# Performance work log

Measured on AMD Instinct MI355X. Metric: run time of the kernel, lower is better.

## Reference

```python
import jax, jax.numpy as jnp
import numpy as np

EMB = 1024
HEADS = 16
HEAD_DIM = EMB // HEADS


def setup_inputs() -> dict:
    key = jax.random.key(0)
    ks = jax.random.split(key, 5)
    x = jax.random.normal(ks[0], (4, 2048, EMB), dtype=jnp.float32)
    # qkv Linear: weight [3*EMB, EMB] in torch; store transposed for x @ W
    Wqkv = jax.random.normal(ks[1], (EMB, 3 * EMB), dtype=jnp.float32) * (1.0 / np.sqrt(EMB))
    bqkv = jax.random.normal(ks[2], (3 * EMB,), dtype=jnp.float32) * 0.01
    Wout = jax.random.normal(ks[3], (EMB, EMB), dtype=jnp.float32) * (1.0 / np.sqrt(EMB))
    bout = jax.random.normal(ks[4], (EMB,), dtype=jnp.float32) * 0.01
    return {"x": x, "Wqkv": Wqkv, "bqkv": bqkv, "Wout": Wout, "bout": bout}


def reference(x, Wqkv, bqkv, Wout, bout):
    B, N, _ = x.shape
    qkv = x @ Wqkv + bqkv                              # [B, N, 3*EMB]
    qkv = qkv.reshape(B, N, 3, HEADS, HEAD_DIM)
    q, k, v = jnp.moveaxis(qkv, 2, 0)                  # each [B, N, H, D]
    q = jnp.swapaxes(q, 1, 2)                          # [B, H, N, D]
    k = jnp.swapaxes(k, 1, 2)
    v = jnp.swapaxes(v, 1, 2)
    scale = 1.0 / np.sqrt(HEAD_DIM).astype(np.float32)
    scores = jnp.einsum('bhqd,bhkd->bhqk', q, k) * scale
    attn = jax.nn.softmax(scores, axis=-1)             # dropout p=0 (eval)
    out = jnp.einsum('bhqk,bhkd->bhqd', attn, v)       # [B, H, N, D]
    out = jnp.swapaxes(out, 1, 2).reshape(B, N, EMB)
    return out @ Wout + bout
```

## Files before the change

### kernel.cpp

```cpp
#include <hip/hip_runtime.h>

#define SEQ   2048
#define EMBD  1024
#define HEADS 16
#define HDIM  64
#define MTOT  8192
#define LOG2E 1.44269504f

typedef __attribute__((ext_vector_type(8))) _Float16 half8;
typedef __attribute__((ext_vector_type(4))) _Float16 half4;
typedef __attribute__((ext_vector_type(2))) __fp16 fp16x2;
typedef __attribute__((ext_vector_type(4))) float f32x4;

__device__ __forceinline__ f32x4 mfma16(half8 a, half8 b, f32x4 c) {
  return __builtin_amdgcn_mfma_f32_16x16x32_f16(a, b, c, 0, 0, 0);
}

__device__ __forceinline__ void gload_lds16(const void* g, void* l) {
  __builtin_amdgcn_global_load_lds(
      (const __attribute__((address_space(1))) unsigned int*)g,
      (__attribute__((address_space(3))) unsigned int*)l, 16, 0, 0);
}

__global__ void k_cvt(const float* __restrict__ in, _Float16* __restrict__ out) {
  size_t i = (size_t)blockIdx.x * blockDim.x + threadIdx.x;
  const f32x4* in4 = (const f32x4*)in;
  f32x4 a = in4[2 * i], b = in4[2 * i + 1];
  half8 h;
  h[0] = (_Float16)a[0]; h[1] = (_Float16)a[1];
  h[2] = (_Float16)a[2]; h[3] = (_Float16)a[3];
  h[4] = (_Float16)b[0]; h[5] = (_Float16)b[1];
  h[6] = (_Float16)b[2]; h[7] = (_Float16)b[3];
  *(half8*)(out + i * 8) = h;
}

__global__ __launch_bounds__(256) void k_transpose(const float* __restrict__ in,
                                                   _Float16* __restrict__ out,
                                                   int R, int C) {
  __shared__ _Float16 tile[64][65];
  const int tid = threadIdx.x;
  const int r0 = blockIdx.y * 64, c0 = blockIdx.x * 64;
  const int tr = tid >> 6;
  const int tc = tid & 63;
  #pragma unroll
  for (int i = 0; i < 16; ++i) {
    const int r = i * 4 + tr;
    tile[r][tc] = (_Float16)in[(size_t)(r0 + r) * C + c0 + tc];
  }
  __syncthreads();
  #pragma unroll
  for (int i = 0; i < 16; ++i) {
    const int cc = i * 4 + tr;
    out[(size_t)(c0 + cc) * R + r0 + tc] = tile[tc][cc];
  }
}

template<int EPI>
__global__ __launch_bounds__(256) void k_gemm(
    const _Float16* __restrict__ A, const _Float16* __restrict__ Bt,
    const float* __restrict__ bias, float* __restrict__ outf,
    _Float16* __restrict__ q, _Float16* __restrict__ k, _Float16* __restrict__ vt)
{
  __shared__ _Float16 sm[2 * 128 * 64];
  _Float16* sA = sm;
  _Float16* sB = sm + 128 * 64;
  const int tid = threadIdx.x;
  const int l = tid & 63, g = l >> 4, c = l & 15;
  const int w = tid >> 6;
  const int wm = (w >> 1) * 64, wn = (w & 1) * 64;
  const int rowBase = blockIdx.y * 128;
  const int colBase = blockIdx.x * 128;

  f32x4 acc[4][4] = {};

  const _Float16* Ag = A + (size_t)(rowBase + (tid >> 3)) * 1024 + (tid & 7) * 8;
  const _Float16* Bg = Bt + (size_t)(colBase + (tid >> 3)) * 1024 + (tid & 7) * 8;
  _Float16* la = sA + tid * 8;
  _Float16* lb = sB + tid * 8;

  for (int kt = 0; kt < 16; ++kt) {
    const _Float16* ag = Ag + kt * 64;
    const _Float16* bg = Bg + kt * 64;
    #pragma unroll
    for (int i = 0; i < 4; ++i) {
      gload_lds16(ag + (size_t)i * 32 * 1024, la + i * 256 * 8);
      gload_lds16(bg + (size_t)i * 32 * 1024, lb + i * 256 * 8);
    }
    __syncthreads();
    #pragma unroll
    for (int kk = 0; kk < 2; ++kk) {
      half8 af[4], bf[4];
      #pragma unroll
      for (int t = 0; t < 4; ++t)
        af[t] = *(const half8*)(sA + (wm + t * 16 + c) * 64 + kk * 32 + g * 8);
      #pragma unroll
      for (int t = 0; t < 4; ++t)
        bf[t] = *(const half8*)(sB + (wn + t * 16 + c) * 64 + kk * 32 + g * 8);
      #pragma unroll
      for (int mt = 0; mt < 4; ++mt)
        #pragma unroll
        for (int nt = 0; nt < 4; ++nt)
          acc[mt][nt] = mfma16(af[mt], bf[nt], acc[mt][nt]);
    }
    __syncthreads();
  }

  #pragma unroll
  for (int mt = 0; mt < 4; ++mt) {
    #pragma unroll
    for (int nt = 0; nt < 4; ++nt) {
      const int col = colBase + wn + nt * 16 + c;
      const float bv = bias[col];
      #pragma unroll
      for (int r = 0; r < 4; ++r) {
        const int row = rowBase + wm + mt * 16 + g * 4 + r;
        const float val = acc[mt][nt][r] + bv;
        if constexpr (EPI == 0) {
          const int s = col >> 10, h = (col >> 6) & 15, d = col & 63;
          const int b = row >> 11, n = row & 2047;
          const int bh = b * HEADS + h;
          const _Float16 hv = (_Float16)val;
          if (s == 2)      vt[((size_t)bh * HDIM + d) * SEQ + n] = hv;
          else if (s == 1) k [((size_t)bh * SEQ + n) * HDIM + d] = hv;
          else             q [((size_t)bh * SEQ + n) * HDIM + d] = hv;
        } else {
          outf[(size_t)row * EMBD + col] = val;
        }
      }
    }
  }
}

__global__ __launch_bounds__(256) void k_attn(
    const _Float16* __restrict__ q, const _Float16* __restrict__ kg,
    const _Float16* __restrict__ vt, _Float16* __restrict__ aout)
{
  __shared__ _Float16 sm[(64 + 64 + 4 * 32) * 72];
  _Float16* Ks = sm;
  _Float16* Vs = sm + 64 * 72;
  const int tid = threadIdx.x;
  const int w = tid >> 6, l = tid & 63, g = l >> 4, c = l & 15;
  _Float16* Pw = sm + 2 * 64 * 72 + w * 32 * 72;
  const int bh = blockIdx.y;
  const int n0 = blockIdx.x * 128 + w * 32;
  const _Float16* qb = q  + (size_t)bh * SEQ * HDIM;
  const _Float16* kb = kg + (size_t)bh * SEQ * HDIM;
  const _Float16* vb = vt + (size_t)bh * HDIM * SEQ;
  const int row0 = tid >> 3, cb = tid & 7;

  half8 aq[2][2];
  #pragma unroll
  for (int qt = 0; qt < 2; ++qt)
    #pragma unroll
    for (int kk = 0; kk < 2; ++kk) {
      half8 t = *(const half8*)(qb + (size_t)(n0 + qt * 16 + c) * HDIM + kk * 32 + g * 8);
      aq[qt][kk] = t * (_Float16)0.125f;
    }

  float m_[2] = {-1e30f, -1e30f};
  float l_[2] = {0.f, 0.f};
  f32x4 o[2][4] = {};

  half8 kr[2], vr[2];
  #pragma unroll
  for (int i = 0; i < 2; ++i) {
    kr[i] = *(const half8*)(kb + (size_t)(i * 256 + tid) * 8);
    vr[i] = *(const half8*)(vb + (size_t)(i * 32 + row0) * SEQ + cb * 8);
  }

  for (int kt = 0; kt < SEQ / 64; ++kt) {
    __syncthreads();
    #pragma unroll
    for (int i = 0; i < 2; ++i) {
      const int row = i * 32 + row0;
      *(half8*)(Ks + row * 72 + cb * 8) = kr[i];
      *(half8*)(Vs + row * 72 + cb * 8) = vr[i];
    }
    if (kt + 1 < SEQ / 64) {
      const _Float16* ksn = kb + (size_t)(kt + 1) * 64 * HDIM;
      #pragma unroll
      for (int i = 0; i < 2; ++i) {
        kr[i] = *(const half8*)(ksn + (size_t)(i * 256 + tid) * 8);
        vr[i] = *(const half8*)(vb + (size_t)(i * 32 + row0) * SEQ + (kt + 1) * 64 + cb * 8);
      }
    }
    __syncthreads();

    f32x4 s[4][2] = {};
    __builtin_amdgcn_s_setprio(1);
    #pragma unroll
    for (int kk = 0; kk < 2; ++kk) {
      #pragma unroll
      for (int kt4 = 0; kt4 < 4; ++kt4) {
        half8 ak = *(const half8*)(Ks + (kt4 * 16 + c) * 72 + kk * 32 + g * 8);
        s[kt4][0] = mfma16(ak, aq[0][kk], s[kt4][0]);
        s[kt4][1] = mfma16(ak, aq[1][kk], s[kt4][1]);
      }
    }
    __builtin_amdgcn_s_setprio(0);

    #pragma unroll
    for (int qf = 0; qf < 2; ++qf) {
      float mx = s[0][qf][0];
      #pragma unroll
      for (int kt4 = 0; kt4 < 4; ++kt4)
        #pragma unroll
        for (int r = 0; r < 4; ++r)
          mx = fmaxf(mx, s[kt4][qf][r]);

      if (__any(mx > m_[qf] + 8.0f)) {
        float fm = fmaxf(mx, __shfl_xor(mx, 16, 64));
        fm = fmaxf(fm, __shfl_xor(fm, 32, 64));
        const float mo = m_[qf];
        const float mn = fmaxf(mo, fm);
        const float cor = __builtin_amdgcn_exp2f((mo - mn) * LOG2E);
        m_[qf] = mn;
        l_[qf] *= cor;
        #pragma unroll
        for (int r = 0; r < 4; ++r) {
          const float corr = __shfl(cor, g * 4 + r, 64);
          #pragma unroll
          for (int dt = 0; dt < 4; ++dt)
            o[qf][dt][r] *= corr;
        }
      }
      const float mn = m_[qf];

      float rs = 0.f;
      _Float16* prow = Pw + (qf * 16 + c) * 72;
      #pragma unroll
      for (int kt4 = 0; kt4 < 4; ++kt4) {
        float p0 = __builtin_amdgcn_exp2f((s[kt4][qf][0] - mn) * LOG2E);
        float p1 = __builtin_amdgcn_exp2f((s[kt4][qf][1] - mn) * LOG2E);
        float p2 = __builtin_amdgcn_exp2f((s[kt4][qf][2] - mn) * LOG2E);
        float p3 = __builtin_amdgcn_exp2f((s[kt4][qf][3] - mn) * LOG2E);
        rs += (p0 + p1) + (p2 + p3);
        union { fp16x2 v2[2]; half4 v4; } u;
        u.v2[0] = __builtin_amdgcn_cvt_pkrtz(p0, p1);
        u.v2[1] = __builtin_amdgcn_cvt_pkrtz(p2, p3);
        *(half4*)(prow + kt4 * 16 + g * 4) = u.v4;
      }
      l_[qf] += rs;
    }

    __builtin_amdgcn_s_setprio(1);
    #pragma unroll
    for (int kk = 0; kk < 2; ++kk) {
      half8 ap0 = *(const half8*)(Pw + (0  + c) * 72 + kk * 32 + g * 8);
      half8 ap1 = *(const half8*)(Pw + (16 + c) * 72 + kk * 32 + g * 8);
      #pragma unroll
      for (int dt = 0; dt < 4; ++dt) {
        half8 bv = *(const half8*)(Vs + (dt * 16 + c) * 72 + kk * 32 + g * 8);
        o[0][dt] = mfma16(ap0, bv, o[0][dt]);
        o[1][dt] = mfma16(ap1, bv, o[1][dt]);
      }
    }
    __builtin_amdgcn_s_setprio(0);
  }

  const int b = bh >> 4, h = bh & 15;
  #pragma unroll
  for (int qt = 0; qt < 2; ++qt) {
    float lt = l_[qt];
    lt += __shfl_xor(lt, 16, 64);
    lt += __shfl_xor(lt, 32, 64);
    #pragma unroll
    for (int r = 0; r < 4; ++r) {
      const float lr = __shfl(lt, g * 4 + r, 64);
      const float rl = __builtin_amdgcn_rcpf(lr);
      const int n = n0 + qt * 16 + g * 4 + r;
      #pragma unroll
      for (int dt = 0; dt < 4; ++dt) {
        aout[((size_t)(b * SEQ + n)) * EMBD + h * HDIM + dt * 16 + c] =
            (_Float16)(o[qt][dt][r] * rl);
      }
    }
  }
}

extern "C" void kernel_launch(void* const* d_in, const int* in_sizes, int n_in,
                              void* d_out, int out_size, void* d_ws, size_t ws_size,
                              hipStream_t stream) {
  const float* x    = (const float*)d_in[0];
  const float* Wqkv = (const float*)d_in[1];
  const float* bqkv = (const float*)d_in[2];
  const float* Wout = (const float*)d_in[3];
  const float* bout = (const float*)d_in[4];
  float* out = (float*)d_out;

  _Float16* ws    = (_Float16*)d_ws;
  _Float16* xh    = ws;
  _Float16* wqkvt = xh + (size_t)MTOT * EMBD;
  _Float16* woutt = wqkvt + (size_t)3 * EMBD * EMBD;
  _Float16* qbuf  = woutt + (size_t)EMBD * EMBD;
  _Float16* kbuf  = qbuf + (size_t)MTOT * EMBD;
  _Float16* vtbuf = kbuf + (size_t)MTOT * EMBD;
  _Float16* aout  = xh;

  k_cvt<<<4096, 256, 0, stream>>>(x, xh);
  k_transpose<<<dim3(48, 16), 256, 0, stream>>>(Wqkv, wqkvt, 1024, 3072);
  k_transpose<<<dim3(16, 16), 256, 0, stream>>>(Wout, woutt, 1024, 1024);
  k_gemm<0><<<dim3(24, 64), 256, 0, stream>>>(xh, wqkvt, bqkv, nullptr,
                                              qbuf, kbuf, vtbuf);
  k_attn<<<dim3(SEQ / 128, 64), 256, 0, stream>>>(qbuf, kbuf, vtbuf, aout);
  k_gemm<1><<<dim3(8, 64), 256, 0, stream>>>(aout, woutt, bout, out,
                                             nullptr, nullptr, nullptr);
}
```

Baseline: 246.6 us.

## Enlarge attention blocks to 8 waves sharing K/V tiles and remap blocks for XCD locality

The attention kernel now runs 512 threads (8 waves) per block covering 256 query rows, so each K/V tile staged in shared memory is reused by twice as many waves and each thread loads only one K and one V vector per step. Block indices are also remapped so that consecutive hardware block IDs, which are spread round-robin across XCDs, map to the same batch-head on a given XCD, improving L2 reuse of K/V. The cost is fewer blocks (512), more shared memory per block, and heavier __syncthreads barriers across 8 waves, which may reduce occupancy and latency hiding.

```diff
diff --git a/kernel.cpp b/kernel.cpp
--- a/kernel.cpp
+++ b/kernel.cpp
@@ -131,18 +131,22 @@
   }
 }
 
-__global__ __launch_bounds__(256) void k_attn(
+__global__ __launch_bounds__(512) void k_attn(
     const _Float16* __restrict__ q, const _Float16* __restrict__ kg,
     const _Float16* __restrict__ vt, _Float16* __restrict__ aout)
 {
-  __shared__ _Float16 sm[(64 + 64 + 4 * 32) * 72];
+  __shared__ _Float16 sm[(64 + 64 + 8 * 32) * 72];
   _Float16* Ks = sm;
   _Float16* Vs = sm + 64 * 72;
   const int tid = threadIdx.x;
   const int w = tid >> 6, l = tid & 63, g = l >> 4, c = l & 15;
   _Float16* Pw = sm + 2 * 64 * 72 + w * 32 * 72;
-  const int bh = blockIdx.y;
-  const int n0 = blockIdx.x * 128 + w * 32;
+
+  const int orig = blockIdx.x;
+  const int lb = (orig & 7) * 64 + (orig >> 3);
+  const int bh = lb >> 3;
+  const int n0 = (lb & 7) * 256 + w * 32;
+
   const _Float16* qb = q  + (size_t)bh * SEQ * HDIM;
   const _Float16* kb = kg + (size_t)bh * SEQ * HDIM;
   const _Float16* vb = vt + (size_t)bh * HDIM * SEQ;
@@ -161,28 +165,16 @@
   float l_[2] = {0.f, 0.f};
   f32x4 o[2][4] = {};
 
-  half8 kr[2], vr[2];
-  #pragma unroll
-  for (int i = 0; i < 2; ++i) {
-    kr[i] = *(const half8*)(kb + (size_t)(i * 256 + tid) * 8);
-    vr[i] = *(const half8*)(vb + (size_t)(i * 32 + row0) * SEQ + cb * 8);
-  }
+  half8 kr = *(const half8*)(kb + (size_t)tid * 8);
+  half8 vr = *(const half8*)(vb + (size_t)row0 * SEQ + cb * 8);
 
   for (int kt = 0; kt < SEQ / 64; ++kt) {
     __syncthreads();
-    #pragma unroll
-    for (int i = 0; i < 2; ++i) {
-      const int row = i * 32 + row0;
-      *(half8*)(Ks + row * 72 + cb * 8) = kr[i];
-      *(half8*)(Vs + row * 72 + cb * 8) = vr[i];
-    }
+    *(half8*)(Ks + row0 * 72 + cb * 8) = kr;
+    *(half8*)(Vs + row0 * 72 + cb * 8) = vr;
     if (kt + 1 < SEQ / 64) {
-      const _Float16* ksn = kb + (size_t)(kt + 1) * 64 * HDIM;
-      #pragma unroll
-      for (int i = 0; i < 2; ++i) {
-        kr[i] = *(const half8*)(ksn + (size_t)(i * 256 + tid) * 8);
-        vr[i] = *(const half8*)(vb + (size_t)(i * 32 + row0) * SEQ + (kt + 1) * 64 + cb * 8);
-      }
+      kr = *(const half8*)(kb + (size_t)(kt + 1) * 64 * HDIM + (size_t)tid * 8);
+      vr = *(const half8*)(vb + (size_t)row0 * SEQ + (kt + 1) * 64 + cb * 8);
     }
     __syncthreads();
 
@@ -302,7 +294,7 @@
   k_transpose<<<dim3(16, 16), 256, 0, stream>>>(Wout, woutt, 1024, 1024);
   k_gemm<0><<<dim3(24, 64), 256, 0, stream>>>(xh, wqkvt, bqkv, nullptr,
                                               qbuf, kbuf, vtbuf);
-  k_attn<<<dim3(SEQ / 128, 64), 256, 0, stream>>>(qbuf, kbuf, vtbuf, aout);
+  k_attn<<<512, 512, 0, stream>>>(qbuf, kbuf, vtbuf, aout);
   k_gemm<1><<<dim3(8, 64), 256, 0, stream>>>(aout, woutt, bout, out,
                                              nullptr, nullptr, nullptr);
 }
```

Result: no change. 242.1 us (-1.8%).
